# Kernel tuning notes

Measured on AMD Instinct MI355X. Metric: run time of the kernel, lower is better.

Reference implementation:

```python
import jax, jax.numpy as jnp
import numpy as np

N, E, EMB, H, HD, T, NG = 2048, 65536, 256, 8, 32, 24, 8


def _linear_params(key, din, dout):
    k1, k2 = jax.random.split(key)
    s = 1.0 / np.sqrt(din)
    W = jax.random.uniform(k1, (din, dout), minval=-s, maxval=s, dtype=jnp.float32)
    b = jax.random.uniform(k2, (dout,), minval=-s, maxval=s, dtype=jnp.float32)
    return W, b


def setup_inputs() -> dict:
    key = jax.random.key(0)
    ks = jax.random.split(key, 16)
    x = jax.random.normal(ks[0], (N, EMB), dtype=jnp.float32)
    edge_index = jax.random.randint(ks[1], (2, E), 0, N, dtype=jnp.int64)
    edge_attr = jax.random.normal(ks[2], (E, 4), dtype=jnp.float32)
    batch = jnp.sort(jax.random.randint(ks[3], (N,), 0, NG, dtype=jnp.int64))
    time_index = jax.random.randint(ks[4], (N,), 0, T, dtype=jnp.int64)
    temporal_embeddings = jax.random.normal(ks[5], (T, EMB), dtype=jnp.float32)
    Wq, bq = _linear_params(ks[6], EMB, EMB)
    Wk, bk = _linear_params(ks[7], EMB, EMB)
    Wv, bv = _linear_params(ks[8], EMB, EMB)
    Wo, bo = _linear_params(ks[9], EMB, EMB)
    We, be = _linear_params(ks[10], 4, H)
    Wtq, btq = _linear_params(ks[11], EMB, EMB)
    Wtk, btk = _linear_params(ks[12], EMB, EMB)
    Wtv, btv = _linear_params(ks[13], EMB, EMB)
    return dict(x=x, edge_index=edge_index, edge_attr=edge_attr, batch=batch,
                time_index=time_index, temporal_embeddings=temporal_embeddings,
                Wq=Wq, bq=bq, Wk=Wk, bk=bk, Wv=Wv, bv=bv, Wo=Wo, bo=bo,
                We=We, be=be, Wtq=Wtq, btq=btq, Wtk=Wtk, btk=btk, Wtv=Wtv, btv=btv)


def _heads(X, n):
    # [n, EMB] -> [H, n, HD]
    return X.reshape(n, H, HD).transpose(1, 0, 2)


def reference(x, edge_index, edge_attr, batch, time_index, temporal_embeddings,
              Wq, bq, Wk, bk, Wv, bv, Wo, bo, We, be, Wtq, btq, Wtk, btk, Wtv, btv):
    n = x.shape[0]
    scale = HD ** -0.5

    Qh = _heads(x @ Wq + bq, n)
    Kh = _heads(x @ Wk + bk, n)
    Vh = _heads(x @ Wv + bv, n)
    scores = jnp.einsum('hnd,hmd->hnm', Qh, Kh) * scale  # [H, n, n]

    # edge bias: vectorized scatter-add of per-edge per-head biases into [H, n, n]
    src, dst = edge_index[0], edge_index[1]
    valid = (src >= 0) & (src < n) & (dst >= 0) & (dst < n)
    eb = edge_attr @ We + be                              # [E, H]
    eb = jnp.where(valid[:, None], eb, 0.0)
    srcc = jnp.clip(src, 0, n - 1)
    dstc = jnp.clip(dst, 0, n - 1)
    scores = scores.at[:, srcc, dstc].add(eb.T)

    # batch mask: nodes may only attend within their own graph
    same_graph = batch[:, None] == batch[None, :]          # [n, n]
    scores = jnp.where(same_graph[None, :, :], scores, -jnp.inf)

    attn = jax.nn.softmax(scores, axis=-1)
    spatial_out = jnp.einsum('hnm,hmd->hnd', attn, Vh)     # [H, n, HD]

    # temporal attention on gathered temporal embeddings
    ti = jnp.clip(time_index, 0, temporal_embeddings.shape[0] - 1)
    emb = temporal_embeddings[ti]                          # [n, EMB]
    TQ = _heads(emb @ Wtq + btq, n)
    TK = _heads(emb @ Wtk + btk, n)
    TV = _heads(emb @ Wtv + btv, n)
    t_scores = jnp.einsum('hnd,hmd->hnm', TQ, TK) * scale
    t_scores = jnp.where(same_graph[None, :, :], t_scores, -jnp.inf)
    t_attn = jax.nn.softmax(t_scores, axis=-1)
    temporal_out = jnp.einsum('hnm,hmd->hnd', t_attn, TV)

    combined = (spatial_out + temporal_out).transpose(1, 0, 2).reshape(n, EMB)
    return combined @ Wo + bo
```

## Files before the change

kernel.cpp:

```cpp
#include <hip/hip_runtime.h>
#include <cstdint>
#include <cstddef>

#define EMB 256
#define NH 8
#define HD 32
#define NG 8
#define TMAX 24

#define LMAX 384
#define LB 384
#define TPB 6
#define VRU 200
#define FM 8.0f

typedef short s16x8 __attribute__((ext_vector_type(8)));
typedef float f32x4 __attribute__((ext_vector_type(4)));

__device__ __forceinline__ unsigned short f2b(float f) {
    unsigned u = __float_as_uint(f);
    return (unsigned short)((u + 0x7FFFu + ((u >> 16) & 1u)) >> 16);
}
__device__ __forceinline__ float b2f(unsigned short h) {
    return __uint_as_float((unsigned)h << 16);
}
__device__ __forceinline__ unsigned long long pack4(unsigned short a, unsigned short b,
                                                    unsigned short c, unsigned short d) {
    return (unsigned long long)a | ((unsigned long long)b << 16) |
           ((unsigned long long)c << 32) | ((unsigned long long)d << 48);
}

__device__ __forceinline__ size_t afrag_idx(int row, int k) {
    return ((size_t)((row >> 4) * 8 + (k >> 5)) << 9) +
           ((((k >> 3) & 3) * 16 + (row & 15)) << 3) + (k & 7);
}

struct PrepArgs {
    float4* Bias4; int bias4;
    const float* x; unsigned short* xh; unsigned short* xl;
    const float* temb; const int* ti; unsigned short* eh; unsigned short* el;
    const float* W[7]; unsigned short* whb; unsigned short* wlb;
    const int* batch; int* gstart; int n;
    int zb, cvtb;
};

__global__ __launch_bounds__(256) void k_prep(PrepArgs pa) {
    __shared__ float tile[32][33];
    int b = blockIdx.x;
    const int t = threadIdx.x;

    if (b < pa.zb) {
        int i = b * 256 + t;
        if (i < pa.bias4) pa.Bias4[i] = make_float4(0.f, 0.f, 0.f, 0.f);
        return;
    }
    b -= pa.zb;
    if (b < pa.cvtb) {
        int i = b * 256 + t;
        if (i < pa.n * (EMB / 4)) {
            int row = i >> 6, k4 = (i & 63) * 4;
            float4 v = ((const float4*)pa.x)[i];
            unsigned short h0 = f2b(v.x), h1 = f2b(v.y), h2 = f2b(v.z), h3 = f2b(v.w);
            size_t o = afrag_idx(row, k4) >> 2;
            ((unsigned long long*)pa.xh)[o] = pack4(h0, h1, h2, h3);
            ((unsigned long long*)pa.xl)[o] = pack4(f2b(v.x - b2f(h0)), f2b(v.y - b2f(h1)),
                                                    f2b(v.z - b2f(h2)), f2b(v.w - b2f(h3)));
        }
        return;
    }
    b -= pa.cvtb;
    if (b < pa.cvtb) {
        int idx = b * 256 + t;
        if (idx < pa.n * (EMB / 4)) {
            int row = idx >> 6, k4 = (idx & 63) * 4;
            int tt = pa.ti[row];
            tt = tt < 0 ? 0 : (tt > TMAX - 1 ? TMAX - 1 : tt);
            float4 v = ((const float4*)pa.temb)[tt * (EMB / 4) + (idx & 63)];
            unsigned short h0 = f2b(v.x), h1 = f2b(v.y), h2 = f2b(v.z), h3 = f2b(v.w);
            size_t o = afrag_idx(row, k4) >> 2;
            ((unsigned long long*)pa.eh)[o] = pack4(h0, h1, h2, h3);
            ((unsigned long long*)pa.el)[o] = pack4(f2b(v.x - b2f(h0)), f2b(v.y - b2f(h1)),
                                                    f2b(v.z - b2f(h2)), f2b(v.w - b2f(h3)));
        }
        return;
    }
    b -= pa.cvtb;
    if (b < 448) {
        const int z = b >> 6, rem = b & 63;
        const int k0 = (rem >> 3) << 5, n0 = (rem & 7) << 5;
        const float* W = pa.W[z];
        unsigned short* Wh = pa.whb + (size_t)z * 65536;
        unsigned short* Wl = pa.wlb + (size_t)z * 65536;
        {
            int rr = t >> 3, c4 = (t & 7) * 4;
            float4 v = *(const float4*)(W + (size_t)(k0 + rr) * 256 + n0 + c4);
            tile[rr][c4 + 0] = v.x; tile[rr][c4 + 1] = v.y;
            tile[rr][c4 + 2] = v.z; tile[rr][c4 + 3] = v.w;
        }
        __syncthreads();
        {
            int nn = n0 + (t >> 3), k4 = (t & 7) * 4;
            float v0 = tile[k4 + 0][t >> 3], v1 = tile[k4 + 1][t >> 3];
            float v2 = tile[k4 + 2][t >> 3], v3 = tile[k4 + 3][t >> 3];
            unsigned short h0 = f2b(v0), h1 = f2b(v1), h2 = f2b(v2), h3 = f2b(v3);
            size_t o = afrag_idx(nn, k0 + k4) >> 2;
            ((unsigned long long*)Wh)[o] = pack4(h0, h1, h2, h3);
            ((unsigned long long*)Wl)[o] = pack4(f2b(v0 - b2f(h0)), f2b(v1 - b2f(h1)),
                                                 f2b(v2 - b2f(h2)), f2b(v3 - b2f(h3)));
        }
        return;
    }
    if (t <= NG) {
        int lo = 0, hi = pa.n;
        while (lo < hi) {
            int mid = (lo + hi) >> 1;
            if (pa.batch[mid] < t) lo = mid + 1; else hi = mid;
        }
        pa.gstart[t] = lo;
    }
}

struct GB {
    const unsigned short* Ah[6];
    const unsigned short* Al[6];
    const float* bias[6];
    unsigned short* Chi[6];
    unsigned short* Clo[6];
    float cscale[6];
};

__global__ __launch_bounds__(256) void k_gemm_split(GB gb,
        const unsigned short* __restrict__ whb, const unsigned short* __restrict__ wlb, int M,
        const int* __restrict__ ei, const float* __restrict__ eattr,
        const float* __restrict__ We, const float* __restrict__ be,
        const int* __restrict__ batch, const int* __restrict__ gstart,
        float* __restrict__ Bias, int E) {
    const int z = blockIdx.z;
    const int t = threadIdx.x;

    if (z == 6) {
        const int stride = gridDim.x * gridDim.y * 256;
        for (int e = (blockIdx.y * gridDim.x + blockIdx.x) * 256 + t; e < E; e += stride) {
            int src = ei[e], dst = ei[E + e];
            if (src < 0 || src >= M || dst < 0 || dst >= M) continue;
            int bs = batch[src];
            if (bs != batch[dst]) continue;
            float4 a = *(const float4*)(eattr + (size_t)e * 4);
            int col = dst - gstart[bs];
#pragma unroll
            for (int h = 0; h < NH; h++) {
                float v = a.x * We[0 * NH + h] + a.y * We[1 * NH + h] +
                          a.z * We[2 * NH + h] + a.w * We[3 * NH + h] + be[h];
                atomicAdd(Bias + ((size_t)h * M + src) * LB + col, v);
            }
        }
        return;
    }

    const unsigned short* Ah = gb.Ah[z];
    const unsigned short* Al = gb.Al[z];
    const unsigned short* Wh = whb + (size_t)z * 65536;
    const unsigned short* Wl = wlb + (size_t)z * 65536;
    const float* bias = gb.bias[z];
    unsigned short* Chi = gb.Chi[z];
    unsigned short* Clo = gb.Clo[z];
    const float cs = gb.cscale[z];
    const bool fs = (Clo != nullptr);

    const int lane = t & 63, wv = t >> 6, lr = lane & 15, lq = lane >> 4;
    const int bm = blockIdx.x * 64 + (wv >> 1) * 32;
    const int bn = blockIdx.y * 64 + (wv & 1) * 32;
    const int mg0 = bm >> 4, ng0 = bn >> 4;

    f32x4 acc[2][2] = {};
#pragma unroll
    for (int kc = 0; kc < 8; kc++) {
        s16x8 ah[2], al[2], bh[2], bl[2];
#pragma unroll
        for (int mi = 0; mi < 2; mi++) {
            size_t o = ((size_t)((mg0 + mi) * 8 + kc) << 9) + lane * 8;
            ah[mi] = *(const s16x8*)(Ah + o);
            if (fs) al[mi] = *(const s16x8*)(Al + o);
        }
#pragma unroll
        for (int ni = 0; ni < 2; ni++) {
            size_t o = ((size_t)((ng0 + ni) * 8 + kc) << 9) + lane * 8;
            bh[ni] = *(const s16x8*)(Wh + o);
            bl[ni] = *(const s16x8*)(Wl + o);
        }
#pragma unroll
        for (int mi = 0; mi < 2; mi++)
#pragma unroll
            for (int ni = 0; ni < 2; ni++) {
                if (fs)
                    acc[mi][ni] = __builtin_amdgcn_mfma_f32_16x16x32_bf16(al[mi], bh[ni], acc[mi][ni], 0, 0, 0);
                acc[mi][ni] = __builtin_amdgcn_mfma_f32_16x16x32_bf16(ah[mi], bl[ni], acc[mi][ni], 0, 0, 0);
                acc[mi][ni] = __builtin_amdgcn_mfma_f32_16x16x32_bf16(ah[mi], bh[ni], acc[mi][ni], 0, 0, 0);
            }
    }
#pragma unroll
    for (int ni = 0; ni < 2; ni++) {
        const int col = bn + ni * 16 + lr;
        const int hh = col >> 5, dd = col & 31;
        float bv = bias[col];
#pragma unroll
        for (int mi = 0; mi < 2; mi++) {
#pragma unroll
            for (int r = 0; r < 4; r++) {
                int crow = bm + mi * 16 + 4 * lq + r;
                if (crow < M) {
                    float val = (acc[mi][ni][r] + bv) * cs;
                    unsigned short h = f2b(val);
                    size_t o = ((size_t)hh * M + crow) * HD + dd;
                    Chi[o] = h;
                    if (fs) Clo[o] = f2b(val - b2f(h));
                }
            }
        }
    }
}

__global__ __launch_bounds__(256) void k_attn5(
    const unsigned short* __restrict__ Qh, const unsigned short* __restrict__ Ql,
    const unsigned short* __restrict__ K, const unsigned short* __restrict__ V,
    const unsigned short* __restrict__ TQh, const unsigned short* __restrict__ TQl,
    const unsigned short* __restrict__ TK, const unsigned short* __restrict__ TV,
    const int* __restrict__ gstart, const float* __restrict__ Bias,
    unsigned short* __restrict__ ch, unsigned short* __restrict__ cl, int n) {

    const int g  = blockIdx.x / TPB;
    const int tp = blockIdx.x % TPB;
    const int h  = blockIdx.y;
    const int gs = gstart[g], ge = gstart[g + 1];
    const int L  = ge - gs;
    const int q0b = tp * 64;
    if (q0b >= L) return;
    const int NC = (L + 31) >> 5;

    __shared__ __align__(16) unsigned int Vt[32 * VRU];
    __shared__ __align__(16) unsigned short Pb[4][16][40];

    const int t = threadIdx.x;
    const int wv = t >> 6, lane = t & 63;
    const int lr = lane & 15, lq = lane >> 4;
    const size_t hb = (size_t)h * n;

    const int q0w = q0b + wv * 16;
    int gq = gs + q0w + lr;
    if (gq > ge - 1) gq = ge - 1;

    float os0[4] = {0.f, 0.f, 0.f, 0.f};
    float os1[4] = {0.f, 0.f, 0.f, 0.f};

    for (int tz = 0; tz < 2; tz++) {
        const unsigned short* Qph = tz ? TQh : Qh;
        const unsigned short* Qpl = tz ? TQl : Ql;
        const unsigned short* Kp  = tz ? TK  : K;
        const unsigned short* Vp  = tz ? TV  : V;
        const bool hasb = (tz == 0);

        if (tz) __syncthreads();

        {
            const int d0 = (t & 7) * 4;
            for (int jp = t >> 3; jp < NC * 16; jp += 32) {
                int j0 = jp * 2;
                unsigned short a0 = 0, a1 = 0, a2 = 0, a3 = 0, b0 = 0, b1 = 0, b2 = 0, b3 = 0;
                if (j0 < L) {
                    const unsigned short* vp = Vp + (hb + gs + j0) * HD + d0;
                    a0 = vp[0]; a1 = vp[1]; a2 = vp[2]; a3 = vp[3];
                }
                if (j0 + 1 < L) {
                    const unsigned short* vp = Vp + (hb + gs + j0 + 1) * HD + d0;
                    b0 = vp[0]; b1 = vp[1]; b2 = vp[2]; b3 = vp[3];
                }
                Vt[(d0 + 0) * VRU + jp] = (unsigned)a0 | ((unsigned)b0 << 16);
                Vt[(d0 + 1) * VRU + jp] = (unsigned)a1 | ((unsigned)b1 << 16);
                Vt[(d0 + 2) * VRU + jp] = (unsigned)a2 | ((unsigned)b2 << 16);
                Vt[(d0 + 3) * VRU + jp] = (unsigned)a3 | ((unsigned)b3 << 16);
            }
        }

        s16x8 qfh = *(const s16x8*)(Qph + (hb + gq) * HD + lq * 8);
        s16x8 qfl = *(const s16x8*)(Qpl + (hb + gq) * HD + lq * 8);
        __syncthreads();

        const float* br0 = Bias; const float* br1 = Bias;
        const float* br2 = Bias; const float* br3 = Bias;
        if (hasb) {
            int r0 = gs + q0w + 4 * lq;
            int a0 = r0 + 0 < n ? r0 + 0 : n - 1;
            int a1 = r0 + 1 < n ? r0 + 1 : n - 1;
            int a2 = r0 + 2 < n ? r0 + 2 : n - 1;
            int a3 = r0 + 3 < n ? r0 + 3 : n - 1;
            br0 = Bias + (hb + a0) * LB;
            br1 = Bias + (hb + a1) * LB;
            br2 = Bias + (hb + a2) * LB;
            br3 = Bias + (hb + a3) * LB;
        }

        auto loadK = [&](int c, int half) -> s16x8 {
            int key = (2 * c + half) * 16 + lr;
            int krow = (key < L) ? (gs + key) : (ge - 1);
            return *(const s16x8*)(Kp + (hb + krow) * HD + lq * 8);
        };

        f32x4 acc0 = {0.f, 0.f, 0.f, 0.f};
        f32x4 acc1 = {0.f, 0.f, 0.f, 0.f};
        float ps0 = 0.f, ps1 = 0.f, ps2 = 0.f, ps3 = 0.f;

        s16x8 kfa = loadK(0, 0), kfb = loadK(0, 1);
        for (int c = 0; c < NC; c++) {
            const int cn = (c + 1 < NC) ? c + 1 : c;
            s16x8 nka = loadK(cn, 0), nkb = loadK(cn, 1);

            float p[2][4];
#pragma unroll
            for (int half = 0; half < 2; half++) {
                const int key = (2 * c + half) * 16 + lr;
                s16x8 kf = half ? kfb : kfa;
                f32x4 d = {0.f, 0.f, 0.f, 0.f};
                d = __builtin_amdgcn_mfma_f32_16x16x32_bf16(qfl, kf, d, 0, 0, 0);
                d = __builtin_amdgcn_mfma_f32_16x16x32_bf16(qfh, kf, d, 0, 0, 0);
                float s0 = d[0], s1 = d[1], s2 = d[2], s3 = d[3];
                if (hasb) {
                    s0 += br0[key]; s1 += br1[key]; s2 += br2[key]; s3 += br3[key];
                }
                const bool ok = key < L;
                s0 = ok ? s0 : -3.0e38f;
                s1 = ok ? s1 : -3.0e38f;
                s2 = ok ? s2 : -3.0e38f;
                s3 = ok ? s3 : -3.0e38f;
                p[half][0] = __expf(s0 - FM);
                p[half][1] = __expf(s1 - FM);
                p[half][2] = __expf(s2 - FM);
                p[half][3] = __expf(s3 - FM);
            }
            ps0 += p[0][0] + p[1][0];
            ps1 += p[0][1] + p[1][1];
            ps2 += p[0][2] + p[1][2];
            ps3 += p[0][3] + p[1][3];
#pragma unroll
            for (int half = 0; half < 2; half++) {
#pragma unroll
                for (int r = 0; r < 4; r++)
                    Pb[wv][4 * lq + r][half * 16 + lr] = f2b(p[half][r]);
            }
            s16x8 pf  = *(const s16x8*)&Pb[wv][lr][8 * lq];
            s16x8 vf0 = *(const s16x8*)&Vt[(size_t)lr * VRU + c * 16 + lq * 4];
            s16x8 vf1 = *(const s16x8*)&Vt[(size_t)(16 + lr) * VRU + c * 16 + lq * 4];
            acc0 = __builtin_amdgcn_mfma_f32_16x16x32_bf16(pf, vf0, acc0, 0, 0, 0);
            acc1 = __builtin_amdgcn_mfma_f32_16x16x32_bf16(pf, vf1, acc1, 0, 0, 0);
            kfa = nka; kfb = nkb;
        }

#pragma unroll
        for (int m = 1; m < 16; m <<= 1) {
            ps0 += __shfl_xor(ps0, m, 16);
            ps1 += __shfl_xor(ps1, m, 16);
            ps2 += __shfl_xor(ps2, m, 16);
            ps3 += __shfl_xor(ps3, m, 16);
        }
        float iv0 = 1.0f / ps0, iv1 = 1.0f / ps1, iv2 = 1.0f / ps2, iv3 = 1.0f / ps3;
        os0[0] += acc0[0] * iv0; os1[0] += acc1[0] * iv0;
        os0[1] += acc0[1] * iv1; os1[1] += acc1[1] * iv1;
        os0[2] += acc0[2] * iv2; os1[2] += acc1[2] * iv2;
        os0[3] += acc0[3] * iv3; os1[3] += acc1[3] * iv3;
    }

    const int qb = q0w + 4 * lq;
#pragma unroll
    for (int r = 0; r < 4; r++) {
        if (qb + r < L) {
            const int grow = gs + qb + r;
            float v0 = os0[r], v1 = os1[r];
            unsigned short h0 = f2b(v0);
            unsigned short l0 = f2b(v0 - b2f(h0));
            unsigned short h1 = f2b(v1);
            unsigned short l1 = f2b(v1 - b2f(h1));
            size_t o0 = afrag_idx(grow, h * HD + lr);
            size_t o1 = afrag_idx(grow, h * HD + 16 + lr);
            ch[o0] = h0; cl[o0] = l0;
            ch[o1] = h1; cl[o1] = l1;
        }
    }
}

__global__ __launch_bounds__(64) void k_gemm_out(const unsigned short* __restrict__ Ah,
        const unsigned short* __restrict__ Al,
        const unsigned short* __restrict__ Wh, const unsigned short* __restrict__ Wl,
        const float* __restrict__ bias, float* __restrict__ C, int M) {
    const int lane = threadIdx.x;
    const int lr = lane & 15, lq = lane >> 4;
    const int bm = blockIdx.x * 16;
    const int bn = blockIdx.y * 32;
    const int mg = bm >> 4, ng0 = bn >> 4;

    f32x4 acc[2] = {};
#pragma unroll
    for (int kc = 0; kc < 8; kc++) {
        size_t oa = ((size_t)(mg * 8 + kc) << 9) + lane * 8;
        s16x8 ah = *(const s16x8*)(Ah + oa);
        s16x8 al = *(const s16x8*)(Al + oa);
#pragma unroll
        for (int ni = 0; ni < 2; ni++) {
            size_t ob = ((size_t)((ng0 + ni) * 8 + kc) << 9) + lane * 8;
            s16x8 bh = *(const s16x8*)(Wh + ob);
            s16x8 bl = *(const s16x8*)(Wl + ob);
            acc[ni] = __builtin_amdgcn_mfma_f32_16x16x32_bf16(al, bh, acc[ni], 0, 0, 0);
            acc[ni] = __builtin_amdgcn_mfma_f32_16x16x32_bf16(ah, bl, acc[ni], 0, 0, 0);
            acc[ni] = __builtin_amdgcn_mfma_f32_16x16x32_bf16(ah, bh, acc[ni], 0, 0, 0);
        }
    }
#pragma unroll
    for (int ni = 0; ni < 2; ni++) {
        const int col = bn + ni * 16 + lr;
        float bv = bias[col];
#pragma unroll
        for (int r = 0; r < 4; r++) {
            const int crow = bm + 4 * lq + r;
            C[(size_t)crow * 256 + col] = acc[ni][r] + bv;
        }
    }
}

extern "C" void kernel_launch(void* const* d_in, const int* in_sizes, int n_in,
                              void* d_out, int out_size, void* d_ws, size_t ws_size,
                              hipStream_t stream) {
    const float* x     = (const float*)d_in[0];
    const int*   ei    = (const int*)d_in[1];
    const float* eattr = (const float*)d_in[2];
    const int*   batch = (const int*)d_in[3];
    const int*   ti    = (const int*)d_in[4];
    const float* temb  = (const float*)d_in[5];
    const float* Wq = (const float*)d_in[6],  *bq = (const float*)d_in[7];
    const float* Wk = (const float*)d_in[8],  *bk = (const float*)d_in[9];
    const float* Wv = (const float*)d_in[10], *bv = (const float*)d_in[11];
    const float* Wo = (const float*)d_in[12], *bo = (const float*)d_in[13];
    const float* We = (const float*)d_in[14], *be = (const float*)d_in[15];
    const float* Wtq = (const float*)d_in[16], *btq = (const float*)d_in[17];
    const float* Wtk = (const float*)d_in[18], *btk = (const float*)d_in[19];
    const float* Wtv = (const float*)d_in[20], *btv = (const float*)d_in[21];

    const int n = in_sizes[0] / EMB;
    const int E = in_sizes[2] / 4;
    float* out = (float*)d_out;

    char* w = (char*)d_ws;
    auto alloc = [&](size_t bytes) -> void* {
        void* p = (void*)w;
        w += (bytes + 255) & ~(size_t)255;
        return p;
    };
    const size_t nb = (size_t)n * EMB * 2;
    unsigned short* xh   = (unsigned short*)alloc(nb);
    unsigned short* xl   = (unsigned short*)alloc(nb);
    unsigned short* eh   = (unsigned short*)alloc(nb);
    unsigned short* el   = (unsigned short*)alloc(nb);
    unsigned short* whb  = (unsigned short*)alloc((size_t)7 * 65536 * 2);
    unsigned short* wlb  = (unsigned short*)alloc((size_t)7 * 65536 * 2);
    unsigned short* Qhb  = (unsigned short*)alloc(nb);
    unsigned short* Qlb  = (unsigned short*)alloc(nb);
    unsigned short* Kb   = (unsigned short*)alloc(nb);
    unsigned short* Vb   = (unsigned short*)alloc(nb);
    unsigned short* TQhb = (unsigned short*)alloc(nb);
    unsigned short* TQlb = (unsigned short*)alloc(nb);
    unsigned short* TKb  = (unsigned short*)alloc(nb);
    unsigned short* TVb  = (unsigned short*)alloc(nb);
    float* Bias  = (float*)alloc((size_t)NH * n * LB * 4);
    unsigned short* ch = (unsigned short*)alloc(nb);
    unsigned short* cl = (unsigned short*)alloc(nb);
    int* gstart  = (int*)alloc((NG + 1) * 4);

    PrepArgs pa;
    pa.Bias4 = (float4*)Bias;
    pa.bias4 = NH * n * LB / 4;
    pa.x = x; pa.xh = xh; pa.xl = xl;
    pa.temb = temb; pa.ti = ti; pa.eh = eh; pa.el = el;
    pa.W[0] = Wq; pa.W[1] = Wk; pa.W[2] = Wv;
    pa.W[3] = Wtq; pa.W[4] = Wtk; pa.W[5] = Wtv; pa.W[6] = Wo;
    pa.whb = whb; pa.wlb = wlb;
    pa.batch = batch; pa.gstart = gstart; pa.n = n;
    pa.zb = (pa.bias4 + 255) / 256;
    pa.cvtb = (n * (EMB / 4) + 255) / 256;
    const int prep_blocks = pa.zb + 2 * pa.cvtb + 448 + 1;
    k_prep<<<dim3(prep_blocks), dim3(256), 0, stream>>>(pa);

    const float scale = 0.17677669529663687f;
    GB gb;
    gb.Ah[0] = xh; gb.Al[0] = xl; gb.bias[0] = bq;  gb.Chi[0] = Qhb;  gb.Clo[0] = Qlb;  gb.cscale[0] = scale;
    gb.Ah[1] = xh; gb.Al[1] = xl; gb.bias[1] = bk;  gb.Chi[1] = Kb;   gb.Clo[1] = nullptr; gb.cscale[1] = 1.f;
    gb.Ah[2] = xh; gb.Al[2] = xl; gb.bias[2] = bv;  gb.Chi[2] = Vb;   gb.Clo[2] = nullptr; gb.cscale[2] = 1.f;
    gb.Ah[3] = eh; gb.Al[3] = el; gb.bias[3] = btq; gb.Chi[3] = TQhb; gb.Clo[3] = TQlb; gb.cscale[3] = scale;
    gb.Ah[4] = eh; gb.Al[4] = el; gb.bias[4] = btk; gb.Chi[4] = TKb;  gb.Clo[4] = nullptr; gb.cscale[4] = 1.f;
    gb.Ah[5] = eh; gb.Al[5] = el; gb.bias[5] = btv; gb.Chi[5] = TVb;  gb.Clo[5] = nullptr; gb.cscale[5] = 1.f;
    k_gemm_split<<<dim3((n + 63) / 64, EMB / 64, 7), dim3(256), 0, stream>>>(
        gb, whb, wlb, n, ei, eattr, We, be, batch, gstart, Bias, E);

    k_attn5<<<dim3(NG * TPB, NH), dim3(256), 0, stream>>>(Qhb, Qlb, Kb, Vb,
                                                          TQhb, TQlb, TKb, TVb,
                                                          gstart, Bias, ch, cl, n);
    k_gemm_out<<<dim3(n / 16, EMB / 32), dim3(64), 0, stream>>>(
        ch, cl, whb + (size_t)6 * 65536, wlb + (size_t)6 * 65536, bo, out, n);
}
```

Baseline: 56.94 us.

## Run spatial and temporal attention concurrently in separate waves of a 512-thread block

The attention kernel now launches 512 threads per block: waves 0-3 compute spatial attention and waves 4-7 compute temporal attention at the same time, instead of one 256-thread block looping over the two passes in sequence. Both V tiles are staged into separate shared buffers up front. The temporal results go through a shared-memory buffer so the spatial waves can add them before writing the combined output. This doubles parallelism per block and removes the serial second pass and its barrier, at the cost of about twice the LDS per block and possibly lower occupancy.

After: 57.49 us. About the same (+1.0%).

```diff
diff --git a/kernel.cpp b/kernel.cpp
--- a/kernel.cpp
+++ b/kernel.cpp
@@ -220,7 +220,7 @@
     }
 }
 
-__global__ __launch_bounds__(256) void k_attn5(
+__global__ __launch_bounds__(512) void k_attn7(
     const unsigned short* __restrict__ Qh, const unsigned short* __restrict__ Ql,
     const unsigned short* __restrict__ K, const unsigned short* __restrict__ V,
     const unsigned short* __restrict__ TQh, const unsigned short* __restrict__ TQl,
@@ -237,151 +237,159 @@
     if (q0b >= L) return;
     const int NC = (L + 31) >> 5;
 
-    __shared__ __align__(16) unsigned int Vt[32 * VRU];
-    __shared__ __align__(16) unsigned short Pb[4][16][40];
+    __shared__ __align__(16) unsigned int Vt[2][32 * VRU];
+    __shared__ __align__(16) unsigned short Pb[8][16][40];
+    __shared__ __align__(16) float Cmb[64][32];
 
     const int t = threadIdx.x;
     const int wv = t >> 6, lane = t & 63;
     const int lr = lane & 15, lq = lane >> 4;
+    const int tz = wv >> 2, w4 = wv & 3;
     const size_t hb = (size_t)h * n;
 
-    const int q0w = q0b + wv * 16;
+    for (int z = 0; z < 2; z++) {
+        const unsigned short* Vp = z ? TV : V;
+        unsigned int* Vz = Vt[z];
+        const int d0 = (t & 7) * 4;
+        for (int jp = t >> 3; jp < NC * 16; jp += 64) {
+            int j0 = jp * 2;
+            unsigned short a0 = 0, a1 = 0, a2 = 0, a3 = 0, b0 = 0, b1 = 0, b2 = 0, b3 = 0;
+            if (j0 < L) {
+                const unsigned short* vp = Vp + (hb + gs + j0) * HD + d0;
+                a0 = vp[0]; a1 = vp[1]; a2 = vp[2]; a3 = vp[3];
+            }
+            if (j0 + 1 < L) {
+                const unsigned short* vp = Vp + (hb + gs + j0 + 1) * HD + d0;
+                b0 = vp[0]; b1 = vp[1]; b2 = vp[2]; b3 = vp[3];
+            }
+            Vz[(d0 + 0) * VRU + jp] = (unsigned)a0 | ((unsigned)b0 << 16);
+            Vz[(d0 + 1) * VRU + jp] = (unsigned)a1 | ((unsigned)b1 << 16);
+            Vz[(d0 + 2) * VRU + jp] = (unsigned)a2 | ((unsigned)b2 << 16);
+            Vz[(d0 + 3) * VRU + jp] = (unsigned)a3 | ((unsigned)b3 << 16);
+        }
+    }
+
+    const unsigned short* Qph = tz ? TQh : Qh;
+    const unsigned short* Qpl = tz ? TQl : Ql;
+    const unsigned short* Kp  = tz ? TK  : K;
+    const unsigned int*   Vz  = Vt[tz];
+    const bool hasb = (tz == 0);
+
+    const int q0w = q0b + w4 * 16;
     int gq = gs + q0w + lr;
     if (gq > ge - 1) gq = ge - 1;
-
-    float os0[4] = {0.f, 0.f, 0.f, 0.f};
-    float os1[4] = {0.f, 0.f, 0.f, 0.f};
-
-    for (int tz = 0; tz < 2; tz++) {
-        const unsigned short* Qph = tz ? TQh : Qh;
-        const unsigned short* Qpl = tz ? TQl : Ql;
-        const unsigned short* Kp  = tz ? TK  : K;
-        const unsigned short* Vp  = tz ? TV  : V;
-        const bool hasb = (tz == 0);
-
-        if (tz) __syncthreads();
-
-        {
-            const int d0 = (t & 7) * 4;
-            for (int jp = t >> 3; jp < NC * 16; jp += 32) {
-                int j0 = jp * 2;
-                unsigned short a0 = 0, a1 = 0, a2 = 0, a3 = 0, b0 = 0, b1 = 0, b2 = 0, b3 = 0;
-                if (j0 < L) {
-                    const unsigned short* vp = Vp + (hb + gs + j0) * HD + d0;
-                    a0 = vp[0]; a1 = vp[1]; a2 = vp[2]; a3 = vp[3];
-                }
-                if (j0 + 1 < L) {
-                    const unsigned short* vp = Vp + (hb + gs + j0 + 1) * HD + d0;
-                    b0 = vp[0]; b1 = vp[1]; b2 = vp[2]; b3 = vp[3];
-                }
-                Vt[(d0 + 0) * VRU + jp] = (unsigned)a0 | ((unsigned)b0 << 16);
-                Vt[(d0 + 1) * VRU + jp] = (unsigned)a1 | ((unsigned)b1 << 16);
-                Vt[(d0 + 2) * VRU + jp] = (unsigned)a2 | ((unsigned)b2 << 16);
-                Vt[(d0 + 3) * VRU + jp] = (unsigned)a3 | ((unsigned)b3 << 16);
-            }
-        }
-
-        s16x8 qfh = *(const s16x8*)(Qph + (hb + gq) * HD + lq * 8);
-        s16x8 qfl = *(const s16x8*)(Qpl + (hb + gq) * HD + lq * 8);
-        __syncthreads();
-
-        const float* br0 = Bias; const float* br1 = Bias;
-        const float* br2 = Bias; const float* br3 = Bias;
-        if (hasb) {
-            int r0 = gs + q0w + 4 * lq;
-            int a0 = r0 + 0 < n ? r0 + 0 : n - 1;
-            int a1 = r0 + 1 < n ? r0 + 1 : n - 1;
-            int a2 = r0 + 2 < n ? r0 + 2 : n - 1;
-            int a3 = r0 + 3 < n ? r0 + 3 : n - 1;
-            br0 = Bias + (hb + a0) * LB;
-            br1 = Bias + (hb + a1) * LB;
-            br2 = Bias + (hb + a2) * LB;
-            br3 = Bias + (hb + a3) * LB;
-        }
-
-        auto loadK = [&](int c, int half) -> s16x8 {
-            int key = (2 * c + half) * 16 + lr;
-            int krow = (key < L) ? (gs + key) : (ge - 1);
-            return *(const s16x8*)(Kp + (hb + krow) * HD + lq * 8);
-        };
-
-        f32x4 acc0 = {0.f, 0.f, 0.f, 0.f};
-        f32x4 acc1 = {0.f, 0.f, 0.f, 0.f};
-        float ps0 = 0.f, ps1 = 0.f, ps2 = 0.f, ps3 = 0.f;
-
-        s16x8 kfa = loadK(0, 0), kfb = loadK(0, 1);
-        for (int c = 0; c < NC; c++) {
-            const int cn = (c + 1 < NC) ? c + 1 : c;
-            s16x8 nka = loadK(cn, 0), nkb = loadK(cn, 1);
-
-            float p[2][4];
-#pragma unroll
-            for (int half = 0; half < 2; half++) {
-                const int key = (2 * c + half) * 16 + lr;
-                s16x8 kf = half ? kfb : kfa;
-                f32x4 d = {0.f, 0.f, 0.f, 0.f};
-                d = __builtin_amdgcn_mfma_f32_16x16x32_bf16(qfl, kf, d, 0, 0, 0);
-                d = __builtin_amdgcn_mfma_f32_16x16x32_bf16(qfh, kf, d, 0, 0, 0);
-                float s0 = d[0], s1 = d[1], s2 = d[2], s3 = d[3];
-                if (hasb) {
-                    s0 += br0[key]; s1 += br1[key]; s2 += br2[key]; s3 += br3[key];
-                }
-                const bool ok = key < L;
-                s0 = ok ? s0 : -3.0e38f;
-                s1 = ok ? s1 : -3.0e38f;
-                s2 = ok ? s2 : -3.0e38f;
-                s3 = ok ? s3 : -3.0e38f;
-                p[half][0] = __expf(s0 - FM);
-                p[half][1] = __expf(s1 - FM);
-                p[half][2] = __expf(s2 - FM);
-                p[half][3] = __expf(s3 - FM);
-            }
-            ps0 += p[0][0] + p[1][0];
-            ps1 += p[0][1] + p[1][1];
-            ps2 += p[0][2] + p[1][2];
-            ps3 += p[0][3] + p[1][3];
-#pragma unroll
-            for (int half = 0; half < 2; half++) {
-#pragma unroll
-                for (int r = 0; r < 4; r++)
-                    Pb[wv][4 * lq + r][half * 16 + lr] = f2b(p[half][r]);
-            }
-            s16x8 pf  = *(const s16x8*)&Pb[wv][lr][8 * lq];
-            s16x8 vf0 = *(const s16x8*)&Vt[(size_t)lr * VRU + c * 16 + lq * 4];
-            s16x8 vf1 = *(const s16x8*)&Vt[(size_t)(16 + lr) * VRU + c * 16 + lq * 4];
-            acc0 = __builtin_amdgcn_mfma_f32_16x16x32_bf16(pf, vf0, acc0, 0, 0, 0);
-            acc1 = __builtin_amdgcn_mfma_f32_16x16x32_bf16(pf, vf1, acc1, 0, 0, 0);
-            kfa = nka; kfb = nkb;
-        }
-
-#pragma unroll
-        for (int m = 1; m < 16; m <<= 1) {
-            ps0 += __shfl_xor(ps0, m, 16);
-            ps1 += __shfl_xor(ps1, m, 16);
-            ps2 += __shfl_xor(ps2, m, 16);
-            ps3 += __shfl_xor(ps3, m, 16);
-        }
-        float iv0 = 1.0f / ps0, iv1 = 1.0f / ps1, iv2 = 1.0f / ps2, iv3 = 1.0f / ps3;
-        os0[0] += acc0[0] * iv0; os1[0] += acc1[0] * iv0;
-        os0[1] += acc0[1] * iv1; os1[1] += acc1[1] * iv1;
-        os0[2] += acc0[2] * iv2; os1[2] += acc1[2] * iv2;
-        os0[3] += acc0[3] * iv3; os1[3] += acc1[3] * iv3;
-    }
-
-    const int qb = q0w + 4 * lq;
-#pragma unroll
-    for (int r = 0; r < 4; r++) {
-        if (qb + r < L) {
-            const int grow = gs + qb + r;
-            float v0 = os0[r], v1 = os1[r];
-            unsigned short h0 = f2b(v0);
-            unsigned short l0 = f2b(v0 - b2f(h0));
-            unsigned short h1 = f2b(v1);
-            unsigned short l1 = f2b(v1 - b2f(h1));
-            size_t o0 = afrag_idx(grow, h * HD + lr);
-            size_t o1 = afrag_idx(grow, h * HD + 16 + lr);
-            ch[o0] = h0; cl[o0] = l0;
-            ch[o1] = h1; cl[o1] = l1;
+    s16x8 qfh = *(const s16x8*)(Qph + (hb + gq) * HD + lq * 8);
+    s16x8 qfl = *(const s16x8*)(Qpl + (hb + gq) * HD + lq * 8);
+    __syncthreads();
+
+    const float* br0 = Bias; const float* br1 = Bias;
+    const float* br2 = Bias; const float* br3 = Bias;
+    if (hasb) {
+        int r0 = gs + q0w + 4 * lq;
+        int a0 = r0 + 0 < n ? r0 + 0 : n - 1;
+        int a1 = r0 + 1 < n ? r0 + 1 : n - 1;
+        int a2 = r0 + 2 < n ? r0 + 2 : n - 1;
+        int a3 = r0 + 3 < n ? r0 + 3 : n - 1;
+        br0 = Bias + (hb + a0) * LB;
+        br1 = Bias + (hb + a1) * LB;
+        br2 = Bias + (hb + a2) * LB;
+        br3 = Bias + (hb + a3) * LB;
+    }
+
+    auto loadK = [&](int c, int half) -> s16x8 {
+        int key = (2 * c + half) * 16 + lr;
+        int krow = (key < L) ? (gs + key) : (ge - 1);
+        return *(const s16x8*)(Kp + (hb + krow) * HD + lq * 8);
+    };
+
+    f32x4 acc0 = {0.f, 0.f, 0.f, 0.f};
+    f32x4 acc1 = {0.f, 0.f, 0.f, 0.f};
+    float ps0 = 0.f, ps1 = 0.f, ps2 = 0.f, ps3 = 0.f;
+
+    s16x8 kfa = loadK(0, 0), kfb = loadK(0, 1);
+    for (int c = 0; c < NC; c++) {
+        const int cn = (c + 1 < NC) ? c + 1 : c;
+        s16x8 nka = loadK(cn, 0), nkb = loadK(cn, 1);
+
+        float p[2][4];
+#pragma unroll
+        for (int half = 0; half < 2; half++) {
+            const int key = (2 * c + half) * 16 + lr;
+            s16x8 kf = half ? kfb : kfa;
+            f32x4 d = {0.f, 0.f, 0.f, 0.f};
+            d = __builtin_amdgcn_mfma_f32_16x16x32_bf16(qfl, kf, d, 0, 0, 0);
+            d = __builtin_amdgcn_mfma_f32_16x16x32_bf16(qfh, kf, d, 0, 0, 0);
+            float s0 = d[0], s1 = d[1], s2 = d[2], s3 = d[3];
+            if (hasb) {
+                s0 += br0[key]; s1 += br1[key]; s2 += br2[key]; s3 += br3[key];
+            }
+            const bool ok = key < L;
+            s0 = ok ? s0 : -3.0e38f;
+            s1 = ok ? s1 : -3.0e38f;
+            s2 = ok ? s2 : -3.0e38f;
+            s3 = ok ? s3 : -3.0e38f;
+            p[half][0] = __expf(s0 - FM);
+            p[half][1] = __expf(s1 - FM);
+            p[half][2] = __expf(s2 - FM);
+            p[half][3] = __expf(s3 - FM);
+        }
+        ps0 += p[0][0] + p[1][0];
+        ps1 += p[0][1] + p[1][1];
+        ps2 += p[0][2] + p[1][2];
+        ps3 += p[0][3] + p[1][3];
+#pragma unroll
+        for (int half = 0; half < 2; half++) {
+#pragma unroll
+            for (int r = 0; r < 4; r++)
+                Pb[wv][4 * lq + r][half * 16 + lr] = f2b(p[half][r]);
+        }
+        s16x8 pf  = *(const s16x8*)&Pb[wv][lr][8 * lq];
+        s16x8 vf0 = *(const s16x8*)&Vz[(size_t)lr * VRU + c * 16 + lq * 4];
+        s16x8 vf1 = *(const s16x8*)&Vz[(size_t)(16 + lr) * VRU + c * 16 + lq * 4];
+        acc0 = __builtin_amdgcn_mfma_f32_16x16x32_bf16(pf, vf0, acc0, 0, 0, 0);
+        acc1 = __builtin_amdgcn_mfma_f32_16x16x32_bf16(pf, vf1, acc1, 0, 0, 0);
+        kfa = nka; kfb = nkb;
+    }
+
+#pragma unroll
+    for (int m = 1; m < 16; m <<= 1) {
+        ps0 += __shfl_xor(ps0, m, 16);
+        ps1 += __shfl_xor(ps1, m, 16);
+        ps2 += __shfl_xor(ps2, m, 16);
+        ps3 += __shfl_xor(ps3, m, 16);
+    }
+    float iv0 = 1.0f / ps0, iv1 = 1.0f / ps1, iv2 = 1.0f / ps2, iv3 = 1.0f / ps3;
+    float os0[4], os1[4];
+    os0[0] = acc0[0] * iv0; os1[0] = acc1[0] * iv0;
+    os0[1] = acc0[1] * iv1; os1[1] = acc1[1] * iv1;
+    os0[2] = acc0[2] * iv2; os1[2] = acc1[2] * iv2;
+    os0[3] = acc0[3] * iv3; os1[3] = acc1[3] * iv3;
+
+    if (tz == 1) {
+#pragma unroll
+        for (int r = 0; r < 4; r++) {
+            Cmb[w4 * 16 + 4 * lq + r][lr]      = os0[r];
+            Cmb[w4 * 16 + 4 * lq + r][16 + lr] = os1[r];
+        }
+    }
+    __syncthreads();
+    if (tz == 0) {
+        const int qb = q0w + 4 * lq;
+#pragma unroll
+        for (int r = 0; r < 4; r++) {
+            if (qb + r < L) {
+                const int grow = gs + qb + r;
+                float v0 = os0[r] + Cmb[w4 * 16 + 4 * lq + r][lr];
+                float v1 = os1[r] + Cmb[w4 * 16 + 4 * lq + r][16 + lr];
+                unsigned short h0 = f2b(v0);
+                unsigned short l0 = f2b(v0 - b2f(h0));
+                unsigned short h1 = f2b(v1);
+                unsigned short l1 = f2b(v1 - b2f(h1));
+                size_t o0 = afrag_idx(grow, h * HD + lr);
+                size_t o1 = afrag_idx(grow, h * HD + 16 + lr);
+                ch[o0] = h0; cl[o0] = l0;
+                ch[o1] = h1; cl[o1] = l1;
+            }
         }
     }
 }
@@ -497,7 +505,7 @@
     k_gemm_split<<<dim3((n + 63) / 64, EMB / 64, 7), dim3(256), 0, stream>>>(
         gb, whb, wlb, n, ei, eattr, We, be, batch, gstart, Bias, E);
 
-    k_attn5<<<dim3(NG * TPB, NH), dim3(256), 0, stream>>>(Qhb, Qlb, Kb, Vb,
+    k_attn7<<<dim3(NG * TPB, NH), dim3(512), 0, stream>>>(Qhb, Qlb, Kb, Vb,
                                                           TQhb, TQlb, TKb, TVb,
                                                           gstart, Bias, ch, cl, n);
     k_gemm_out<<<dim3(n / 16, EMB / 32), dim3(64), 0, stream>>>(
```
